# Performance work log

Hardware: AMD Instinct MI355X
Metric: run time of the kernel (lower is better)

The kernel has to match this reference:

```python
import jax, jax.numpy as jnp
import numpy as np

N, E, F, H, C, G = 100000, 1600000, 128, 128, 1, 512
NLAYERS, DT, ALPHA, GAMMA = 5, 1.0, 1.0, 1.0


def setup_inputs() -> dict:
    key = jax.random.key(0)
    ks = jax.random.split(key, 11)
    x = jax.random.normal(ks[0], (N, F), dtype=jnp.float32)
    edge_index = jax.random.randint(ks[1], (2, E), 0, N, dtype=jnp.int64)
    batch = jnp.sort(jax.random.randint(ks[2], (N,), 0, G, dtype=jnp.int64))
    s = 1.0 / np.sqrt(H).astype(np.float32)
    W_enc = jax.random.normal(ks[3], (H, F), jnp.float32) * (1.0 / np.sqrt(F))
    b_enc = jnp.zeros((H,), jnp.float32)
    W_conv = jax.random.normal(ks[4], (H, H), jnp.float32) * s
    b_conv = jnp.zeros((H,), jnp.float32)
    W_res = jax.random.normal(ks[5], (H, H), jnp.float32) * s
    b_res = jnp.zeros((H,), jnp.float32)
    W_dec = jax.random.normal(ks[6], (C, H), jnp.float32) * s
    b_dec = jnp.zeros((C,), jnp.float32)
    return {
        "x": x, "edge_index": edge_index, "batch": batch,
        "W_enc": W_enc, "b_enc": b_enc,
        "W_conv": W_conv, "b_conv": b_conv,
        "W_res": W_res, "b_res": b_res,
        "W_dec": W_dec, "b_dec": b_dec,
    }


def reference(x, edge_index, batch, W_enc, b_enc, W_conv, b_conv, W_res, b_res, W_dec, b_dec):
    src, dst = edge_index[0], edge_index[1]
    # GCN symmetric normalization with self-loops: deg = 1 + in-degree(dst)
    deg = jnp.zeros((N,), x.dtype).at[dst].add(1.0) + 1.0
    dinv = jax.lax.rsqrt(deg)
    norm = dinv[src] * dinv[dst]            # [E]
    self_norm = (dinv * dinv)[:, None]      # [N,1] self-loop coefficient

    def gcn_conv(X):
        xw = X @ W_conv.T                   # lin (bias=False)
        agg = jnp.zeros_like(xw).at[dst].add(norm[:, None] * xw[src])
        agg = agg + self_norm * xw          # self-loop term
        return agg + b_conv

    Y = x @ W_enc.T + b_enc
    Xs = Y
    for _ in range(NLAYERS):
        res = Xs @ W_res.T + b_res - Xs @ W_conv.T   # res(X) - conv.lin(X)
        Y = Y + DT * (jax.nn.relu(gcn_conv(Xs) + res) - ALPHA * Y - GAMMA * Xs)
        Xs = Xs + DT * Y
    out = Xs @ W_dec.T + b_dec               # [N, 1]
    pooled = jax.ops.segment_sum(out, batch, num_segments=G)  # [G, 1]
    return pooled.squeeze(-1)                # [G]
```

## Files before the change

### kernel.cpp

```cpp
#include <hip/hip_runtime.h>
#include <hip/hip_bf16.h>
#include <stdint.h>


#define HD 128
#define SCHUNK 2048

typedef __attribute__((ext_vector_type(4))) float f32x4;
typedef __attribute__((ext_vector_type(8))) float f32x8;
typedef __attribute__((ext_vector_type(8))) _Float16 f16x8;

__global__ __launch_bounds__(256) void k_deg(const int* __restrict__ dst, int E,
                                             int* __restrict__ cnt){
  int e = blockIdx.x * 256 + threadIdx.x;
  if (e < E) atomicAdd(&cnt[dst[e]], 1);
}

__global__ __launch_bounds__(256) void k_scan_part(const int* __restrict__ cnt,
                                                   int* __restrict__ bsum, int N){
  __shared__ int red[256];
  int t = threadIdx.x;
  int lo = blockIdx.x * SCHUNK + t * 8;
  int s = 0;
#pragma unroll
  for (int k = 0; k < 8; ++k){
    int i = lo + k;
    s += (i < N) ? cnt[i] : 0;
  }
  red[t] = s;
  __syncthreads();
  for (int off = 128; off > 0; off >>= 1){
    if (t < off) red[t] += red[t + off];
    __syncthreads();
  }
  if (t == 0) bsum[blockIdx.x] = red[0];
}

__global__ __launch_bounds__(1024) void k_scan_mid(const int* __restrict__ bsum,
                                                   int* __restrict__ boff, int nb,
                                                   int* __restrict__ rp, int N, int E){
  __shared__ int part[1024];
  int t = threadIdx.x;
  part[t] = (t < nb) ? bsum[t] : 0;
  __syncthreads();
  for (int off = 1; off < 1024; off <<= 1){
    int v = (t >= off) ? part[t - off] : 0;
    __syncthreads();
    part[t] += v;
    __syncthreads();
  }
  if (t < nb) boff[t] = (t == 0) ? 0 : part[t - 1];
  if (t == 0) rp[N] = E;
}

__global__ __launch_bounds__(256) void k_scan_apply(const int* __restrict__ cnt,
                                                    const int* __restrict__ boff,
                                                    int* __restrict__ rp,
                                                    float* __restrict__ dinv, int N){
  __shared__ int tsum[256];
  int t = threadIdx.x;
  int lo = blockIdx.x * SCHUNK + t * 8;
  int v[8];
  int s = 0;
#pragma unroll
  for (int k = 0; k < 8; ++k){
    int i = lo + k;
    v[k] = (i < N) ? cnt[i] : 0;
    s += v[k];
  }
  tsum[t] = s;
  __syncthreads();
  for (int off = 1; off < 256; off <<= 1){
    int u = (t >= off) ? tsum[t - off] : 0;
    __syncthreads();
    tsum[t] += u;
    __syncthreads();
  }
  int base = boff[blockIdx.x] + ((t == 0) ? 0 : tsum[t - 1]);
#pragma unroll
  for (int k = 0; k < 8; ++k){
    int i = lo + k;
    if (i < N){
      rp[i] = base;
      dinv[i] = rsqrtf((float)v[k] + 1.0f);
      base += v[k];
    }
  }
}

__global__ __launch_bounds__(256) void k_fill(const int* __restrict__ src,
                                              const int* __restrict__ dst, int E,
                                              const int* __restrict__ rp,
                                              int* cnt,
                                              const float* __restrict__ dinv,
                                              unsigned* __restrict__ col){
  int e = blockIdx.x * 256 + threadIdx.x;
  if (e >= E) return;
  int s = src[e], d = dst[e];
  int pos = rp[d] + atomicSub(&cnt[d], 1) - 1;
  float di = dinv[s];
  int deg1 = (int)(1.0f / (di * di) + 0.5f);
  col[pos] = ((unsigned)deg1 << 18) | (unsigned)s;
}

__global__ __launch_bounds__(256) void k_prep_w(const float* __restrict__ Wc,
                                                const float* __restrict__ Wr,
                                                const float* __restrict__ We,
                                                const float* __restrict__ bc,
                                                const float* __restrict__ br,
                                                _Float16* __restrict__ WcF,
                                                _Float16* __restrict__ WrF,
                                                _Float16* __restrict__ WeF,
                                                float* __restrict__ bias_sum){
  int i = blockIdx.x * 256 + threadIdx.x;
  if (i < HD * HD){
    WcF[i] = (_Float16)Wc[i];
    WrF[i] = (_Float16)Wr[i];
    WeF[i] = (_Float16)We[i];
  }
  if (i < HD) bias_sum[i] = bc[i] + br[i];
}

__global__ __launch_bounds__(256) void k_agg(const _Float16* __restrict__ XsH,
                                             const float* __restrict__ dinv,
                                             const int* __restrict__ rp,
                                             const unsigned* __restrict__ col,
                                             _Float16* __restrict__ U,
                                             int N){
  int w = threadIdx.x >> 6;
  int lane = threadIdx.x & 63;
  int q = lane >> 4;
  int ql = lane & 15;
  int node = blockIdx.x * 4 + w;
  if (node >= N) return;

  float acc[8];
#pragma unroll
  for (int i = 0; i < 8; ++i) acc[i] = 0.f;

  int b = rp[node], e = rp[node + 1];
  int j = b + q;
  for (; j + 4 < e; j += 8){
    unsigned r0 = col[j];
    unsigned r1 = col[j + 4];
    float w0 = rsqrtf((float)(r0 >> 18));
    float w1 = rsqrtf((float)(r1 >> 18));
    f16x8 v0 = ((const f16x8*)(XsH + (size_t)(r0 & 0x3FFFFu) * HD))[ql];
    f16x8 v1 = ((const f16x8*)(XsH + (size_t)(r1 & 0x3FFFFu) * HD))[ql];
#pragma unroll
    for (int i = 0; i < 8; ++i) acc[i] = fmaf(w0, (float)v0[i], acc[i]);
#pragma unroll
    for (int i = 0; i < 8; ++i) acc[i] = fmaf(w1, (float)v1[i], acc[i]);
  }
  if (j < e){
    unsigned r0 = col[j];
    float w0 = rsqrtf((float)(r0 >> 18));
    f16x8 v0 = ((const f16x8*)(XsH + (size_t)(r0 & 0x3FFFFu) * HD))[ql];
#pragma unroll
    for (int i = 0; i < 8; ++i) acc[i] = fmaf(w0, (float)v0[i], acc[i]);
  }

  float dn = dinv[node];
#pragma unroll
  for (int i = 0; i < 8; ++i){
    acc[i] += __shfl_xor(acc[i], 16, 64);
    acc[i] += __shfl_xor(acc[i], 32, 64);
    acc[i] *= dn;
  }
  if (q == 0){
    f16x8 o;
#pragma unroll
    for (int i = 0; i < 8; ++i) o[i] = (_Float16)acc[i];
    ((f16x8*)(U + (size_t)node * HD))[ql] = o;
  }
}

__global__ __launch_bounds__(256) void k_gemm(
    const float* __restrict__ A1f,
    const _Float16* __restrict__ A1h,
    const _Float16* A2h,
    const _Float16* __restrict__ W1,
    const _Float16* __restrict__ W2,
    const float* __restrict__ dinvp,
    const float* __restrict__ bias,
    _Float16* outXsH,
    const float* __restrict__ Wd, const float* __restrict__ bd,
    float* __restrict__ val,
    int N, int relu, int decode){
  __shared__ _Float16 wsm[2 * HD * HD];
  f16x8* smv = (f16x8*)wsm;

  {
    int t = threadIdx.x;
    const f16x8* g1 = (const f16x8*)W1;
    for (int i = t; i < HD * HD / 8; i += 256){
      int row = i >> 4, slot = i & 15;
      smv[(row << 4) | (slot ^ (row & 7))] = g1[i];
    }
    if (W2){
      const f16x8* g2 = (const f16x8*)W2;
      for (int i = t; i < HD * HD / 8; i += 256){
        int row = i >> 4, slot = i & 15;
        smv[2048 + ((row << 4) | (slot ^ (row & 7)))] = g2[i];
      }
    }
  }
  __syncthreads();

  int wid = blockIdx.x * 4 + (threadIdx.x >> 6);
  int row0 = wid * 32;
  if (row0 >= N) return;
  int lane = threadIdx.x & 63;
  int r = lane & 15;
  int kg = lane >> 4;

  f32x4 acc[2][8];
#pragma unroll
  for (int s = 0; s < 2; ++s)
#pragma unroll
    for (int c = 0; c < 8; ++c) acc[s][c] = (f32x4)0.0f;

  const bool two = (A2h != nullptr);
  float sr[2] = {0.f, 0.f};
  if (two){
#pragma unroll
    for (int s = 0; s < 2; ++s){
      float d = dinvp[row0 + s * 16 + r];
      sr[s] = d * d - 1.0f;
    }
  }

#pragma unroll
  for (int kst = 0; kst < 4; ++kst){
    int k0 = kst * 32 + kg * 8;
    f16x8 a1[2], a2[2];
#pragma unroll
    for (int s = 0; s < 2; ++s){
      size_t ao = (size_t)(row0 + s * 16 + r) * HD + k0;
      if (two){
        f16x8 uh = *(const f16x8*)(A1h + ao);
        f16x8 xv = *(const f16x8*)(A2h + ao);
        a2[s] = xv;
#pragma unroll
        for (int i = 0; i < 8; ++i)
          a1[s][i] = (_Float16)fmaf(sr[s], (float)xv[i], (float)uh[i]);
      } else {
        f32x8 u = *(const f32x8*)(A1f + ao);
#pragma unroll
        for (int i = 0; i < 8; ++i) a1[s][i] = (_Float16)u[i];
      }
    }
    int swz = (kst * 4 + kg) ^ (r & 7);
#pragma unroll
    for (int ct = 0; ct < 8; ++ct){
      int ridx = ((ct * 16 + r) << 4) | swz;
      f16x8 b1 = smv[ridx];
#pragma unroll
      for (int s = 0; s < 2; ++s)
        acc[s][ct] = __builtin_amdgcn_mfma_f32_16x16x32_f16(a1[s], b1, acc[s][ct], 0, 0, 0);
      if (two){
        f16x8 b2 = smv[2048 + ridx];
#pragma unroll
        for (int s = 0; s < 2; ++s)
          acc[s][ct] = __builtin_amdgcn_mfma_f32_16x16x32_f16(a2[s], b2, acc[s][ct], 0, 0, 0);
      }
    }
  }

  float rowp[2][4] = {{0.f,0.f,0.f,0.f},{0.f,0.f,0.f,0.f}};
#pragma unroll
  for (int s = 0; s < 2; ++s){
#pragma unroll
    for (int ct = 0; ct < 8; ++ct){
      int cc = ct * 16 + r;
      float bv = bias[cc];
      float wdv = decode ? Wd[cc] : 0.f;
#pragma unroll
      for (int j = 0; j < 4; ++j){
        float v = acc[s][ct][j] + bv;
        if (relu) v = fmaxf(v, 0.0f);
        if (decode){
          rowp[s][j] += v * wdv;
        } else {
          int rr = row0 + s * 16 + kg * 4 + j;
          outXsH[(size_t)rr * HD + cc] = (_Float16)v;
        }
      }
    }
  }
  if (decode){
    float bd0 = bd[0];
#pragma unroll
    for (int s = 0; s < 2; ++s)
#pragma unroll
      for (int j = 0; j < 4; ++j){
        float t = rowp[s][j];
        t += __shfl_xor(t, 1, 64);
        t += __shfl_xor(t, 2, 64);
        t += __shfl_xor(t, 4, 64);
        t += __shfl_xor(t, 8, 64);
        if (r == 0) val[row0 + s * 16 + kg * 4 + j] = t + bd0;
      }
  }
}

#define POOL_CHUNK 1024
__global__ __launch_bounds__(256) void k_pool(const float* __restrict__ val,
                                              const int* __restrict__ batch,
                                              float* __restrict__ out, int N, int G){
  __shared__ float acc[4096];
  int t = threadIdx.x;
  int lo = blockIdx.x * POOL_CHUNK;
  int hi = min(lo + POOL_CHUNK, N);
  if (G <= 4096){
    for (int i = t; i < G; i += 256) acc[i] = 0.f;
    __syncthreads();
    for (int i = lo + t; i < hi; i += 256) atomicAdd(&acc[batch[i]], val[i]);
    __syncthreads();
    for (int i = t; i < G; i += 256){
      float v = acc[i];
      if (v != 0.f) atomicAdd(&out[i], v);
    }
  } else {
    for (int i = lo + t; i < hi; i += 256) atomicAdd(&out[batch[i]], val[i]);
  }
}

extern "C" void kernel_launch(void* const* d_in, const int* in_sizes, int n_in,
                              void* d_out, int out_size, void* d_ws, size_t ws_size,
                              hipStream_t stream){
  const float* x      = (const float*)d_in[0];
  const int*   ei     = (const int*)d_in[1];
  const int*   batch  = (const int*)d_in[2];
  const float* W_enc  = (const float*)d_in[3];
  const float* b_enc  = (const float*)d_in[4];
  const float* W_conv = (const float*)d_in[5];
  const float* b_conv = (const float*)d_in[6];
  const float* W_res  = (const float*)d_in[7];
  const float* b_res  = (const float*)d_in[8];
  const float* W_dec  = (const float*)d_in[9];
  const float* b_dec  = (const float*)d_in[10];

  const int N = in_sizes[0] / HD;
  const int E = in_sizes[1] / 2;
  float* out = (float*)d_out;

  char* ws = (char*)d_ws;
  size_t off = 0;
  auto alloc = [&](size_t bytes) -> char* {
    char* p = ws + off;
    off += (bytes + 255) & ~(size_t)255;
    return p;
  };
  int*   cnt   = (int*)  alloc((size_t)N * 4);
  int*   rp    = (int*)  alloc(((size_t)N + 1) * 4);
  float* dinv  = (float*)alloc((size_t)N * 4);
  int*   bsum  = (int*)  alloc(1024 * 4);
  int*   boff  = (int*)  alloc(1024 * 4);
  unsigned* col= (unsigned*)alloc((size_t)E * 4);
  _Float16* XsH= (_Float16*)alloc((size_t)N * HD * 2);
  _Float16* U  = (_Float16*)alloc((size_t)N * HD * 2);
  float* val   = (float*)alloc((size_t)N * 4);
  _Float16* WcF = (_Float16*)alloc((size_t)HD * HD * 2);
  _Float16* WrF = (_Float16*)alloc((size_t)HD * HD * 2);
  _Float16* WeF = (_Float16*)alloc((size_t)HD * HD * 2);
  float* bias_sum = (float*)alloc((size_t)HD * 4);

  hipMemsetAsync(cnt, 0, (size_t)N * 4, stream);
  hipMemsetAsync(out, 0, (size_t)out_size * 4, stream);

  const int* src = ei;
  const int* dst = ei + E;

  int nb = (N + SCHUNK - 1) / SCHUNK;

  k_deg       <<<(E + 255) / 256, 256, 0, stream>>>(dst, E, cnt);
  k_scan_part <<<nb, 256, 0, stream>>>(cnt, bsum, N);
  k_scan_mid  <<<1, 1024, 0, stream>>>(bsum, boff, nb, rp, N, E);
  k_scan_apply<<<nb, 256, 0, stream>>>(cnt, boff, rp, dinv, N);
  k_fill      <<<(E + 255) / 256, 256, 0, stream>>>(src, dst, E, rp, cnt, dinv, col);
  k_prep_w    <<<(HD * HD + 255) / 256, 256, 0, stream>>>(W_conv, W_res, W_enc, b_conv, b_res,
                                                          WcF, WrF, WeF, bias_sum);

  int gemm_blocks = ((N + 31) / 32 + 3) / 4;
  int node_blocks = (N + 3) / 4;

  k_gemm<<<gemm_blocks, 256, 0, stream>>>(x, nullptr, nullptr, WeF, nullptr,
                                          nullptr, b_enc, XsH,
                                          nullptr, nullptr, nullptr, N, 0, 0);

  for (int l = 0; l < 5; ++l){
    k_agg<<<node_blocks, 256, 0, stream>>>(XsH, dinv, rp, col, U, N);
    int last = (l == 4);
    k_gemm<<<gemm_blocks, 256, 0, stream>>>(nullptr, U, XsH, WcF, WrF,
                                            dinv, bias_sum, XsH,
                                            W_dec, b_dec, val, N, 1, last);
  }

  k_pool<<<(N + POOL_CHUNK - 1) / POOL_CHUNK, 256, 0, stream>>>(val, batch, out, N, out_size);
}
```

Measured before the change: 643.6 us.

## Partition CSR build atomics into destination ranges and unroll aggregation loop

The degree count and CSR fill kernels become grid-stride loops that make four passes over the edge list. Each pass only handles edges whose destination falls in one quarter of the node range, which keeps the atomic targets and row pointer reads within a smaller, more cache-resident window. The price is reading dst four times. Separately, the aggregation gather loop is unrolled from two to four neighbours per iteration to keep more loads in flight, with the tail now handled by a loop.

Result: no change. 653.4 us (+1.5%).

```diff
diff --git a/kernel.cpp b/kernel.cpp
--- a/kernel.cpp
+++ b/kernel.cpp
@@ -5,15 +5,25 @@
 
 #define HD 128
 #define SCHUNK 2048
+#define CSR_ROUNDS 4
+#define CSR_GRID 2048
 
 typedef __attribute__((ext_vector_type(4))) float f32x4;
 typedef __attribute__((ext_vector_type(8))) float f32x8;
 typedef __attribute__((ext_vector_type(8))) _Float16 f16x8;
 
 __global__ __launch_bounds__(256) void k_deg(const int* __restrict__ dst, int E,
-                                             int* __restrict__ cnt){
-  int e = blockIdx.x * 256 + threadIdx.x;
-  if (e < E) atomicAdd(&cnt[dst[e]], 1);
+                                             int* __restrict__ cnt, int N){
+  int tid = blockIdx.x * 256 + threadIdx.x;
+  int stride = gridDim.x * 256;
+  int seg = (N + CSR_ROUNDS - 1) / CSR_ROUNDS;
+  for (int r = 0; r < CSR_ROUNDS; ++r){
+    int lo = r * seg, hi = min(lo + seg, N);
+    for (int e = tid; e < E; e += stride){
+      int d = dst[e];
+      if (d >= lo && d < hi) atomicAdd(&cnt[d], 1);
+    }
+  }
 }
 
 __global__ __launch_bounds__(256) void k_scan_part(const int* __restrict__ cnt,
@@ -93,14 +103,23 @@
                                               const int* __restrict__ rp,
                                               int* cnt,
                                               const float* __restrict__ dinv,
-                                              unsigned* __restrict__ col){
-  int e = blockIdx.x * 256 + threadIdx.x;
-  if (e >= E) return;
-  int s = src[e], d = dst[e];
-  int pos = rp[d] + atomicSub(&cnt[d], 1) - 1;
-  float di = dinv[s];
-  int deg1 = (int)(1.0f / (di * di) + 0.5f);
-  col[pos] = ((unsigned)deg1 << 18) | (unsigned)s;
+                                              unsigned* __restrict__ col, int N){
+  int tid = blockIdx.x * 256 + threadIdx.x;
+  int stride = gridDim.x * 256;
+  int seg = (N + CSR_ROUNDS - 1) / CSR_ROUNDS;
+  for (int r = 0; r < CSR_ROUNDS; ++r){
+    int lo = r * seg, hi = min(lo + seg, N);
+    for (int e = tid; e < E; e += stride){
+      int d = dst[e];
+      if (d >= lo && d < hi){
+        int s = src[e];
+        int pos = rp[d] + atomicSub(&cnt[d], 1) - 1;
+        float di = dinv[s];
+        int deg1 = (int)(1.0f / (di * di) + 0.5f);
+        col[pos] = ((unsigned)deg1 << 18) | (unsigned)s;
+      }
+    }
+  }
 }
 
 __global__ __launch_bounds__(256) void k_prep_w(const float* __restrict__ Wc,
@@ -140,19 +159,29 @@
 
   int b = rp[node], e = rp[node + 1];
   int j = b + q;
-  for (; j + 4 < e; j += 8){
+  for (; j + 12 < e; j += 16){
     unsigned r0 = col[j];
     unsigned r1 = col[j + 4];
+    unsigned r2 = col[j + 8];
+    unsigned r3 = col[j + 12];
     float w0 = rsqrtf((float)(r0 >> 18));
     float w1 = rsqrtf((float)(r1 >> 18));
+    float w2 = rsqrtf((float)(r2 >> 18));
+    float w3 = rsqrtf((float)(r3 >> 18));
     f16x8 v0 = ((const f16x8*)(XsH + (size_t)(r0 & 0x3FFFFu) * HD))[ql];
     f16x8 v1 = ((const f16x8*)(XsH + (size_t)(r1 & 0x3FFFFu) * HD))[ql];
+    f16x8 v2 = ((const f16x8*)(XsH + (size_t)(r2 & 0x3FFFFu) * HD))[ql];
+    f16x8 v3 = ((const f16x8*)(XsH + (size_t)(r3 & 0x3FFFFu) * HD))[ql];
 #pragma unroll
     for (int i = 0; i < 8; ++i) acc[i] = fmaf(w0, (float)v0[i], acc[i]);
 #pragma unroll
     for (int i = 0; i < 8; ++i) acc[i] = fmaf(w1, (float)v1[i], acc[i]);
-  }
-  if (j < e){
+#pragma unroll
+    for (int i = 0; i < 8; ++i) acc[i] = fmaf(w2, (float)v2[i], acc[i]);
+#pragma unroll
+    for (int i = 0; i < 8; ++i) acc[i] = fmaf(w3, (float)v3[i], acc[i]);
+  }
+  for (; j < e; j += 4){
     unsigned r0 = col[j];
     float w0 = rsqrtf((float)(r0 >> 18));
     f16x8 v0 = ((const f16x8*)(XsH + (size_t)(r0 & 0x3FFFFu) * HD))[ql];
@@ -374,11 +403,11 @@
 
   int nb = (N + SCHUNK - 1) / SCHUNK;
 
-  k_deg       <<<(E + 255) / 256, 256, 0, stream>>>(dst, E, cnt);
+  k_deg       <<<CSR_GRID, 256, 0, stream>>>(dst, E, cnt, N);
   k_scan_part <<<nb, 256, 0, stream>>>(cnt, bsum, N);
   k_scan_mid  <<<1, 1024, 0, stream>>>(bsum, boff, nb, rp, N, E);
   k_scan_apply<<<nb, 256, 0, stream>>>(cnt, boff, rp, dinv, N);
-  k_fill      <<<(E + 255) / 256, 256, 0, stream>>>(src, dst, E, rp, cnt, dinv, col);
+  k_fill      <<<CSR_GRID, 256, 0, stream>>>(src, dst, E, rp, cnt, dinv, col, N);
   k_prep_w    <<<(HD * HD + 255) / 256, 256, 0, stream>>>(W_conv, W_res, W_enc, b_conv, b_res,
                                                           WcF, WrF, WeF, bias_sum);
 
```

## Halve GEMM shared-memory weights by staging W2 after W1, unroll SpMM gather

Applied to the files above, without the earlier changes.

The GEMM kernel now keeps a single 32KB weight buffer in LDS instead of 64KB. It runs the W1 pass first, then reloads the buffer with W2 behind extra barriers and runs the second MFMA pass. Inactive waves stay alive, clamped to row 0, so they can take part in the barriers. The aim is higher occupancy from lower LDS use, at the cost of an extra weight reload, two more barriers and a second read of A2 per block. The SpMM gather loop is also unrolled to four neighbours per iteration, giving more memory-level parallelism.

Result: no change. 648.8 us (+0.8%).

```diff
diff --git a/kernel.cpp b/kernel.cpp
--- a/kernel.cpp
+++ b/kernel.cpp
@@ -140,19 +140,29 @@
 
   int b = rp[node], e = rp[node + 1];
   int j = b + q;
-  for (; j + 4 < e; j += 8){
+  for (; j + 12 < e; j += 16){
     unsigned r0 = col[j];
     unsigned r1 = col[j + 4];
+    unsigned r2 = col[j + 8];
+    unsigned r3 = col[j + 12];
     float w0 = rsqrtf((float)(r0 >> 18));
     float w1 = rsqrtf((float)(r1 >> 18));
+    float w2 = rsqrtf((float)(r2 >> 18));
+    float w3 = rsqrtf((float)(r3 >> 18));
     f16x8 v0 = ((const f16x8*)(XsH + (size_t)(r0 & 0x3FFFFu) * HD))[ql];
     f16x8 v1 = ((const f16x8*)(XsH + (size_t)(r1 & 0x3FFFFu) * HD))[ql];
+    f16x8 v2 = ((const f16x8*)(XsH + (size_t)(r2 & 0x3FFFFu) * HD))[ql];
+    f16x8 v3 = ((const f16x8*)(XsH + (size_t)(r3 & 0x3FFFFu) * HD))[ql];
 #pragma unroll
     for (int i = 0; i < 8; ++i) acc[i] = fmaf(w0, (float)v0[i], acc[i]);
 #pragma unroll
     for (int i = 0; i < 8; ++i) acc[i] = fmaf(w1, (float)v1[i], acc[i]);
-  }
-  if (j < e){
+#pragma unroll
+    for (int i = 0; i < 8; ++i) acc[i] = fmaf(w2, (float)v2[i], acc[i]);
+#pragma unroll
+    for (int i = 0; i < 8; ++i) acc[i] = fmaf(w3, (float)v3[i], acc[i]);
+  }
+  for (; j < e; j += 4){
     unsigned r0 = col[j];
     float w0 = rsqrtf((float)(r0 >> 18));
     f16x8 v0 = ((const f16x8*)(XsH + (size_t)(r0 & 0x3FFFFu) * HD))[ql];
@@ -187,30 +197,24 @@
     const float* __restrict__ Wd, const float* __restrict__ bd,
     float* __restrict__ val,
     int N, int relu, int decode){
-  __shared__ _Float16 wsm[2 * HD * HD];
+  __shared__ _Float16 wsm[HD * HD];
   f16x8* smv = (f16x8*)wsm;
+  int t = threadIdx.x;
 
   {
-    int t = threadIdx.x;
     const f16x8* g1 = (const f16x8*)W1;
     for (int i = t; i < HD * HD / 8; i += 256){
       int row = i >> 4, slot = i & 15;
       smv[(row << 4) | (slot ^ (row & 7))] = g1[i];
     }
-    if (W2){
-      const f16x8* g2 = (const f16x8*)W2;
-      for (int i = t; i < HD * HD / 8; i += 256){
-        int row = i >> 4, slot = i & 15;
-        smv[2048 + ((row << 4) | (slot ^ (row & 7)))] = g2[i];
-      }
-    }
   }
   __syncthreads();
 
-  int wid = blockIdx.x * 4 + (threadIdx.x >> 6);
+  int wid = blockIdx.x * 4 + (t >> 6);
   int row0 = wid * 32;
-  if (row0 >= N) return;
-  int lane = threadIdx.x & 63;
+  bool act = (row0 < N);
+  int rowb = act ? row0 : 0;
+  int lane = t & 63;
   int r = lane & 15;
   int kg = lane >> 4;
 
@@ -225,7 +229,7 @@
   if (two){
 #pragma unroll
     for (int s = 0; s < 2; ++s){
-      float d = dinvp[row0 + s * 16 + r];
+      float d = dinvp[rowb + s * 16 + r];
       sr[s] = d * d - 1.0f;
     }
   }
@@ -233,14 +237,13 @@
 #pragma unroll
   for (int kst = 0; kst < 4; ++kst){
     int k0 = kst * 32 + kg * 8;
-    f16x8 a1[2], a2[2];
+    f16x8 a1[2];
 #pragma unroll
     for (int s = 0; s < 2; ++s){
-      size_t ao = (size_t)(row0 + s * 16 + r) * HD + k0;
+      size_t ao = (size_t)(rowb + s * 16 + r) * HD + k0;
       if (two){
         f16x8 uh = *(const f16x8*)(A1h + ao);
         f16x8 xv = *(const f16x8*)(A2h + ao);
-        a2[s] = xv;
 #pragma unroll
         for (int i = 0; i < 8; ++i)
           a1[s][i] = (_Float16)fmaf(sr[s], (float)xv[i], (float)uh[i]);
@@ -253,13 +256,34 @@
     int swz = (kst * 4 + kg) ^ (r & 7);
 #pragma unroll
     for (int ct = 0; ct < 8; ++ct){
-      int ridx = ((ct * 16 + r) << 4) | swz;
-      f16x8 b1 = smv[ridx];
+      f16x8 b1 = smv[((ct * 16 + r) << 4) | swz];
 #pragma unroll
       for (int s = 0; s < 2; ++s)
         acc[s][ct] = __builtin_amdgcn_mfma_f32_16x16x32_f16(a1[s], b1, acc[s][ct], 0, 0, 0);
-      if (two){
-        f16x8 b2 = smv[2048 + ridx];
+    }
+  }
+
+  if (two){
+    __syncthreads();
+    const f16x8* g2 = (const f16x8*)W2;
+    for (int i = t; i < HD * HD / 8; i += 256){
+      int row = i >> 4, slot = i & 15;
+      smv[(row << 4) | (slot ^ (row & 7))] = g2[i];
+    }
+    __syncthreads();
+#pragma unroll
+    for (int kst = 0; kst < 4; ++kst){
+      int k0 = kst * 32 + kg * 8;
+      f16x8 a2[2];
+#pragma unroll
+      for (int s = 0; s < 2; ++s){
+        size_t ao = (size_t)(rowb + s * 16 + r) * HD + k0;
+        a2[s] = *(const f16x8*)(A2h + ao);
+      }
+      int swz = (kst * 4 + kg) ^ (r & 7);
+#pragma unroll
+      for (int ct = 0; ct < 8; ++ct){
+        f16x8 b2 = smv[((ct * 16 + r) << 4) | swz];
 #pragma unroll
         for (int s = 0; s < 2; ++s)
           acc[s][ct] = __builtin_amdgcn_mfma_f32_16x16x32_f16(a2[s], b2, acc[s][ct], 0, 0, 0);
@@ -281,25 +305,25 @@
         if (relu) v = fmaxf(v, 0.0f);
         if (decode){
           rowp[s][j] += v * wdv;
-        } else {
+        } else if (act){
           int rr = row0 + s * 16 + kg * 4 + j;
           outXsH[(size_t)rr * HD + cc] = (_Float16)v;
         }
       }
     }
   }
-  if (decode){
+  if (decode && act){
     float bd0 = bd[0];
 #pragma unroll
     for (int s = 0; s < 2; ++s)
 #pragma unroll
       for (int j = 0; j < 4; ++j){
-        float t = rowp[s][j];
-        t += __shfl_xor(t, 1, 64);
-        t += __shfl_xor(t, 2, 64);
-        t += __shfl_xor(t, 4, 64);
-        t += __shfl_xor(t, 8, 64);
-        if (r == 0) val[row0 + s * 16 + kg * 4 + j] = t + bd0;
+        float tt = rowp[s][j];
+        tt += __shfl_xor(tt, 1, 64);
+        tt += __shfl_xor(tt, 2, 64);
+        tt += __shfl_xor(tt, 4, 64);
+        tt += __shfl_xor(tt, 8, 64);
+        if (r == 0) val[row0 + s * 16 + kg * 4 + j] = tt + bd0;
       }
   }
 }
```
